# Optimization experiments

Measured on AMD Instinct MI355X. Metric: run time of the kernel, lower is better.

The kernel has to match this reference:

```python
import jax, jax.numpy as jnp
import numpy as np

N = 8192
E = 262144
H = 64


def setup_inputs() -> dict:
    key = jax.random.key(0)
    ks = jax.random.split(key, 9)
    edge_index = jax.random.randint(ks[0], (2, E), 0, N, dtype=jnp.int64)
    edge_attr = jax.random.uniform(ks[1], (E,), dtype=jnp.float32)
    node_features = jax.random.normal(ks[2], (N, N), dtype=jnp.float32)
    # GCNConv weights (glorot-ish scale) and biases
    W1 = jax.random.normal(ks[3], (N, H), dtype=jnp.float32) / np.sqrt(N)
    b1 = jnp.zeros((H,), dtype=jnp.float32)
    W2 = jax.random.normal(ks[4], (H, H), dtype=jnp.float32) / np.sqrt(H)
    b2 = jnp.zeros((H,), dtype=jnp.float32)
    fcW = jax.random.normal(ks[5], (H, N), dtype=jnp.float32) / np.sqrt(H)
    fcb = jnp.zeros((N,), dtype=jnp.float32)
    return {"edge_index": edge_index, "edge_attr": edge_attr,
            "node_features": node_features,
            "W1": W1, "b1": b1, "W2": W2, "b2": b2,
            "fcW": fcW, "fcb": fcb}


def _gcn_conv(x, W, b, src, dst, ew, n_nodes):
    # PyG GCNConv with edge weights: x' = D^{-1/2} (A + I) D^{-1/2} (x W) + b
    # src/dst/ew already include self-loops (weight 1.0).
    x = x @ W                                        # [N, out]
    deg = jax.ops.segment_sum(ew, dst, num_segments=n_nodes)  # in-degree w/ loops
    dinv = jax.lax.rsqrt(deg)                        # deg >= 1 due to self loops
    norm = dinv[src] * ew * dinv[dst]                # [E+N]
    out = jax.ops.segment_sum(x[src] * norm[:, None], dst, num_segments=n_nodes)
    return out + b


def reference(edge_index, edge_attr, node_features, W1, b1, W2, b2, fcW, fcb):
    n_nodes = node_features.shape[0]
    loops = jnp.arange(n_nodes, dtype=edge_index.dtype)
    src = jnp.concatenate([edge_index[0], loops])
    dst = jnp.concatenate([edge_index[1], loops])
    ew = jnp.concatenate([edge_attr, jnp.ones((n_nodes,), edge_attr.dtype)])
    x = jax.nn.relu(_gcn_conv(node_features, W1, b1, src, dst, ew, n_nodes))
    x = jax.nn.relu(_gcn_conv(x, W2, b2, src, dst, ew, n_nodes))
    x = x @ fcW + fcb
    return jax.nn.softmax(x, axis=-1)
```

## Files before the change

kernel.cpp:

```cpp
#include <hip/hip_runtime.h>


#define NN 8192
#define NE 262144
#define HD 64

typedef float f32x4 __attribute__((ext_vector_type(4)));
typedef short v8s   __attribute__((ext_vector_type(8)));
typedef unsigned short ushort_t;

__device__ __forceinline__ unsigned short bf16_rne(float f){
  union { float f; unsigned u; } v; v.f = f;
  unsigned r = v.u + 0x7fffu + ((v.u >> 16) & 1u);
  return (unsigned short)(r >> 16);
}
__device__ __forceinline__ float bf16_f32(unsigned short h){
  union { unsigned u; float f; } v; v.u = ((unsigned)h) << 16;
  return v.f;
}
__device__ __forceinline__ f32x4 mfma16(v8s a, v8s b, f32x4 c){
  return __builtin_amdgcn_mfma_f32_16x16x32_bf16(a, b, c, 0, 0, 0);
}

__global__ void k_init(float* deg, int* cnt, int* wcnt, float* S){
  int i = blockIdx.x*blockDim.x + threadIdx.x;
  if (i < NN){ deg[i]=1.0f; cnt[i]=0; wcnt[i]=0; S[i]=0.0f; }
}

__global__ void k_deg_cnt(const int* ei, const float* ew, float* deg, int* cnt){
  int e = blockIdx.x*blockDim.x + threadIdx.x;
  if (e < NE){
    int d = ei[NE + e];
    atomicAdd(&deg[d], ew[e]);
    atomicAdd(&cnt[d], 1);
  }
}

__global__ void k_dinv(const float* deg, float* dinv){
  int i = blockIdx.x*blockDim.x + threadIdx.x;
  if (i < NN) dinv[i] = 1.0f / sqrtf(deg[i]);
}

__global__ void k_scan(const int* cnt, int* rowptr){
  __shared__ int part[256];
  int t = threadIdx.x;
  int loc[32]; int s = 0;
  #pragma unroll
  for (int j=0;j<32;++j){ loc[j] = cnt[t*32+j]; s += loc[j]; }
  part[t] = s; __syncthreads();
  for (int off=1; off<256; off<<=1){
    int v = (t >= off) ? part[t-off] : 0;
    __syncthreads();
    part[t] += v;
    __syncthreads();
  }
  int run = part[t] - s;
  #pragma unroll
  for (int j=0;j<32;++j){ rowptr[t*32+j] = run; run += loc[j]; }
  if (t == 255) rowptr[NN] = run;
}

__global__ void k_fill(const int* ei, const float* ew, const float* dinv,
                       const int* rowptr, int* wcnt, int* csr_src, float* csr_nrm){
  int e = blockIdx.x*blockDim.x + threadIdx.x;
  if (e < NE){
    int s = ei[e], d = ei[NE+e];
    int slot = rowptr[d] + atomicAdd(&wcnt[d], 1);
    csr_src[slot] = s;
    csr_nrm[slot] = dinv[s] * ew[e] * dinv[d];
  }
}

__global__ void k_pack_w1(const float* W1, ushort_t* w1hi, ushort_t* w1lo){
  int idx = blockIdx.x*blockDim.x + threadIdx.x;
  if (idx < NN*HD){
    int kk = idx & 31, c = (idx>>5)&15, nt = (idx>>9)&3, kb = idx>>11;
    int k = kb*32 + kk, col = nt*16 + c;
    float w = W1[(size_t)k*HD + col];
    unsigned short hi = bf16_rne(w);
    w1hi[idx] = hi;
    w1lo[idx] = bf16_rne(w - bf16_f32(hi));
  }
}

__global__ void k_pack_fcw(const float* fcW, ushort_t* fcwp){
  int idx = blockIdx.x*blockDim.x + threadIdx.x;
  if (idx < HD*NN){
    int kk = idx & 31, c = (idx>>5)&15, cblk = (idx>>9)&511, kb = idx>>18;
    int k = kb*32 + kk, col = cblk*16 + c;
    fcwp[idx] = bf16_rne(fcW[(size_t)k*NN + col]);
  }
}

__global__ __launch_bounds__(512) void k_gemm1(const float* __restrict__ X,
                                               const ushort_t* __restrict__ w1hi,
                                               const ushort_t* __restrict__ w1lo,
                                               float* __restrict__ xw1){
  int tid = threadIdx.x, lane = tid & 63, w = tid >> 6;
  int r = lane & 15, seg = lane >> 4;
  int row0 = blockIdx.x * 32;
  const float* xr0 = X + (size_t)(row0 + r)     * NN + seg*8;
  const float* xr1 = X + (size_t)(row0 + 16 + r)* NN + seg*8;
  int kbase = w * 1024;

  f32x4 z = {0.f,0.f,0.f,0.f};
  f32x4 acc0[4] = {z,z,z,z};
  f32x4 acc1[4] = {z,z,z,z};

  f32x4 p00 = *(const f32x4*)(xr0 + kbase);
  f32x4 p01 = *(const f32x4*)(xr0 + kbase + 4);
  f32x4 p10 = *(const f32x4*)(xr1 + kbase);
  f32x4 p11 = *(const f32x4*)(xr1 + kbase + 4);

  for (int it = 0; it < 32; ++it){
    int k0 = kbase + it*32;
    int kb = k0 >> 5;
    f32x4 c00=p00, c01=p01, c10=p10, c11=p11;
    if (it < 31){
      int kn = k0 + 32;
      p00 = *(const f32x4*)(xr0 + kn);
      p01 = *(const f32x4*)(xr0 + kn + 4);
      p10 = *(const f32x4*)(xr1 + kn);
      p11 = *(const f32x4*)(xr1 + kn + 4);
    }
    v8s a0h, a0l, a1h, a1l;
    #pragma unroll
    for (int j=0;j<4;++j){
      float f = c00[j]; unsigned short h = bf16_rne(f);
      a0h[j] = (short)h; a0l[j] = (short)bf16_rne(f - bf16_f32(h));
      f = c01[j]; h = bf16_rne(f);
      a0h[4+j] = (short)h; a0l[4+j] = (short)bf16_rne(f - bf16_f32(h));
      f = c10[j]; h = bf16_rne(f);
      a1h[j] = (short)h; a1l[j] = (short)bf16_rne(f - bf16_f32(h));
      f = c11[j]; h = bf16_rne(f);
      a1h[4+j] = (short)h; a1l[4+j] = (short)bf16_rne(f - bf16_f32(h));
    }
    #pragma unroll
    for (int nt=0; nt<4; ++nt){
      size_t boff = ((size_t)(kb*4 + nt)*16 + r)*32 + seg*8;
      v8s bh = *(const v8s*)(w1hi + boff);
      v8s bl = *(const v8s*)(w1lo + boff);
      acc0[nt] = mfma16(a0h, bh, acc0[nt]);
      acc0[nt] = mfma16(a0h, bl, acc0[nt]);
      acc0[nt] = mfma16(a0l, bh, acc0[nt]);
      acc1[nt] = mfma16(a1h, bh, acc1[nt]);
      acc1[nt] = mfma16(a1h, bl, acc1[nt]);
      acc1[nt] = mfma16(a1l, bh, acc1[nt]);
    }
  }

  __shared__ float red[8][32][64];
  #pragma unroll
  for (int nt=0; nt<4; ++nt)
    #pragma unroll
    for (int j=0;j<4;++j){
      red[w][4*seg + j][nt*16 + r]      = acc0[nt][j];
      red[w][16 + 4*seg + j][nt*16 + r] = acc1[nt][j];
    }
  __syncthreads();
  for (int o = tid; o < 32*64; o += 512){
    int rr = o >> 6, cc = o & 63;
    float s = 0.f;
    #pragma unroll
    for (int ww=0; ww<8; ++ww) s += red[ww][rr][cc];
    xw1[(size_t)(row0 + rr)*HD + cc] = s;
  }
}

__global__ __launch_bounds__(256) void k_agg(const float* __restrict__ xin,
                                             const float* __restrict__ bias,
                                             const float* __restrict__ dinv,
                                             const int* __restrict__ rowptr,
                                             const int* __restrict__ csr_src,
                                             const float* __restrict__ csr_nrm,
                                             float* outf, ushort_t* outb, int mode){
  int lane = threadIdx.x & 63, w = threadIdx.x >> 6;
  int i = blockIdx.x*4 + w;
  float di = dinv[i];
  float acc = di*di * xin[(size_t)i*HD + lane];
  int e = rowptr[i], e1 = rowptr[i+1];
  for (; e + 1 < e1; e += 2){
    int s0 = csr_src[e], s1 = csr_src[e+1];
    float n0 = csr_nrm[e], n1 = csr_nrm[e+1];
    acc += n0 * xin[(size_t)s0*HD + lane];
    acc += n1 * xin[(size_t)s1*HD + lane];
  }
  if (e < e1) acc += csr_nrm[e] * xin[(size_t)csr_src[e]*HD + lane];
  float v = acc + bias[lane];
  v = v > 0.f ? v : 0.f;
  if (mode == 0) outf[(size_t)i*HD + lane] = v;
  else           outb[(size_t)i*HD + lane] = bf16_rne(v);
}

__global__ __launch_bounds__(64) void k_conv2(const float* __restrict__ x1a,
                                              const float* __restrict__ W2,
                                              float* __restrict__ x2w){
  int i = blockIdx.x, h = threadIdx.x;
  __shared__ float xs[64];
  xs[h] = x1a[(size_t)i*HD + h];
  __syncthreads();
  float acc = 0.f;
  #pragma unroll
  for (int k=0;k<64;++k) acc += xs[k] * W2[k*HD + h];
  x2w[(size_t)i*HD + h] = acc;
}

__global__ __launch_bounds__(256) void k_rowsum(const ushort_t* __restrict__ x2b,
                                                const ushort_t* __restrict__ fcwp,
                                                const float* __restrict__ fcb,
                                                float* __restrict__ S){
  int lane = threadIdx.x & 63, w = threadIdx.x >> 6;
  int r = lane & 15, seg = lane >> 4;
  int row0 = blockIdx.x*128 + w*32;
  const ushort_t* xb = x2b + (size_t)(row0 + r)*HD + seg*8;
  v8s a00 = *(const v8s*)(xb);
  v8s a01 = *(const v8s*)(xb + 32);
  v8s a10 = *(const v8s*)(xb + 16*HD);
  v8s a11 = *(const v8s*)(xb + 16*HD + 32);
  float rp0[4] = {0,0,0,0}, rp1[4] = {0,0,0,0};
  for (int cb=0; cb<4; ++cb){
    int colbase = blockIdx.y*256 + cb*64;
    f32x4 z = {0.f,0.f,0.f,0.f};
    f32x4 acc0[4] = {z,z,z,z}, acc1[4] = {z,z,z,z};
    #pragma unroll
    for (int nt=0; nt<4; ++nt){
      int cblk = (colbase >> 4) + nt;
      v8s bA = *(const v8s*)(fcwp + ((size_t)cblk*16 + r)*32 + seg*8);
      v8s bB = *(const v8s*)(fcwp + ((size_t)(512 + cblk)*16 + r)*32 + seg*8);
      acc0[nt] = mfma16(a00, bA, acc0[nt]);
      acc0[nt] = mfma16(a01, bB, acc0[nt]);
      acc1[nt] = mfma16(a10, bA, acc1[nt]);
      acc1[nt] = mfma16(a11, bB, acc1[nt]);
    }
    #pragma unroll
    for (int nt=0; nt<4; ++nt){
      int col = colbase + nt*16 + r;
      float fb = fcb[col];
      #pragma unroll
      for (int j=0;j<4;++j){
        rp0[j] += __expf(acc0[nt][j] + fb);
        rp1[j] += __expf(acc1[nt][j] + fb);
      }
    }
  }
  #pragma unroll
  for (int m=1; m<16; m<<=1)
    #pragma unroll
    for (int j=0;j<4;++j){
      rp0[j] += __shfl_xor(rp0[j], m);
      rp1[j] += __shfl_xor(rp1[j], m);
    }
  if (r == 0){
    #pragma unroll
    for (int j=0;j<4;++j){
      atomicAdd(&S[row0 + 4*seg + j],      rp0[j]);
      atomicAdd(&S[row0 + 16 + 4*seg + j], rp1[j]);
    }
  }
}

__global__ void k_sinv(const float* S, float* Sinv){
  int i = blockIdx.x*blockDim.x + threadIdx.x;
  if (i < NN) Sinv[i] = 1.0f / S[i];
}

__global__ __launch_bounds__(256) void k_passB(const ushort_t* __restrict__ x2b,
                                               const ushort_t* __restrict__ fcwp,
                                               const float* __restrict__ fcb,
                                               const float* __restrict__ Sinv,
                                               float* __restrict__ out){
  int lane = threadIdx.x & 63, w = threadIdx.x >> 6;
  int r = lane & 15, seg = lane >> 4;
  int row0 = blockIdx.x*128 + w*32;
  const ushort_t* xb = x2b + (size_t)(row0 + r)*HD + seg*8;
  v8s a00 = *(const v8s*)(xb);
  v8s a01 = *(const v8s*)(xb + 32);
  v8s a10 = *(const v8s*)(xb + 16*HD);
  v8s a11 = *(const v8s*)(xb + 16*HD + 32);
  float si0[4], si1[4];
  #pragma unroll
  for (int j=0;j<4;++j){
    si0[j] = Sinv[row0 + 4*seg + j];
    si1[j] = Sinv[row0 + 16 + 4*seg + j];
  }
  for (int cb=0; cb<4; ++cb){
    int colbase = blockIdx.y*256 + cb*64;
    f32x4 z = {0.f,0.f,0.f,0.f};
    f32x4 acc0[4] = {z,z,z,z}, acc1[4] = {z,z,z,z};
    #pragma unroll
    for (int nt=0; nt<4; ++nt){
      int cblk = (colbase >> 4) + nt;
      v8s bA = *(const v8s*)(fcwp + ((size_t)cblk*16 + r)*32 + seg*8);
      v8s bB = *(const v8s*)(fcwp + ((size_t)(512 + cblk)*16 + r)*32 + seg*8);
      acc0[nt] = mfma16(a00, bA, acc0[nt]);
      acc0[nt] = mfma16(a01, bB, acc0[nt]);
      acc1[nt] = mfma16(a10, bA, acc1[nt]);
      acc1[nt] = mfma16(a11, bB, acc1[nt]);
    }
    #pragma unroll
    for (int nt=0; nt<4; ++nt){
      int col = colbase + nt*16 + r;
      float fb = fcb[col];
      #pragma unroll
      for (int j=0;j<4;++j){
        out[(size_t)(row0 + 4*seg + j)*NN + col]      = __expf(acc0[nt][j] + fb) * si0[j];
        out[(size_t)(row0 + 16 + 4*seg + j)*NN + col] = __expf(acc1[nt][j] + fb) * si1[j];
      }
    }
  }
}

extern "C" void kernel_launch(void* const* d_in, const int* in_sizes, int n_in,
                              void* d_out, int out_size, void* d_ws, size_t ws_size,
                              hipStream_t stream){
  (void)in_sizes; (void)n_in; (void)out_size; (void)ws_size;
  const int*   ei  = (const int*)  d_in[0];
  const float* ew  = (const float*)d_in[1];
  const float* X   = (const float*)d_in[2];
  const float* W1  = (const float*)d_in[3];
  const float* b1  = (const float*)d_in[4];
  const float* W2  = (const float*)d_in[5];
  const float* b2  = (const float*)d_in[6];
  const float* fcW = (const float*)d_in[7];
  const float* fcb = (const float*)d_in[8];
  float* out = (float*)d_out;
  char*  ws  = (char*)d_ws;

  float*    deg     = (float*)   (ws + 0);
  float*    dinv    = (float*)   (ws + 32768);
  int*      cnt     = (int*)     (ws + 65536);
  int*      wcnt    = (int*)     (ws + 98304);
  int*      rowptr  = (int*)     (ws + 131072);
  int*      csr_src = (int*)     (ws + 167936);
  float*    csr_nrm = (float*)   (ws + 1216512);
  ushort_t* w1hi    = (ushort_t*)(ws + 2265088);
  ushort_t* w1lo    = (ushort_t*)(ws + 3313664);
  ushort_t* fcwp    = (ushort_t*)(ws + 4362240);
  float*    xw1     = (float*)   (ws + 5410816);
  float*    x1a     = (float*)   (ws + 7507968);
  float*    x2w     = (float*)   (ws + 9605120);
  ushort_t* x2b     = (ushort_t*)(ws + 11702272);
  float*    S       = (float*)   (ws + 12750848);
  float*    Sinv    = (float*)   (ws + 12783616);

  k_init    <<<32,   256, 0, stream>>>(deg, cnt, wcnt, S);
  k_deg_cnt <<<1024, 256, 0, stream>>>(ei, ew, deg, cnt);
  k_dinv    <<<32,   256, 0, stream>>>(deg, dinv);
  k_scan    <<<1,    256, 0, stream>>>(cnt, rowptr);
  k_fill    <<<1024, 256, 0, stream>>>(ei, ew, dinv, rowptr, wcnt, csr_src, csr_nrm);
  k_pack_w1 <<<2048, 256, 0, stream>>>(W1, w1hi, w1lo);
  k_pack_fcw<<<2048, 256, 0, stream>>>(fcW, fcwp);
  k_gemm1   <<<256,  512, 0, stream>>>(X, w1hi, w1lo, xw1);
  k_agg     <<<2048, 256, 0, stream>>>(xw1, b1, dinv, rowptr, csr_src, csr_nrm, x1a, (ushort_t*)0, 0);
  k_conv2   <<<8192,  64, 0, stream>>>(x1a, W2, x2w);
  k_agg     <<<2048, 256, 0, stream>>>(x2w, b2, dinv, rowptr, csr_src, csr_nrm, (float*)0, x2b, 1);
  k_rowsum  <<<dim3(64,32), 256, 0, stream>>>(x2b, fcwp, fcb, S);
  k_sinv    <<<32,   256, 0, stream>>>(S, Sinv);
  k_passB   <<<dim3(64,32), 256, 0, stream>>>(x2b, fcwp, fcb, Sinv, out);
}
```

Baseline: 301.4 us.

## Fuse small kernels, transpose MFMA operands for vectorized softmax stores

```diff
diff --git a/kernel.cpp b/kernel.cpp
--- a/kernel.cpp
+++ b/kernel.cpp
@@ -22,9 +22,24 @@
   return __builtin_amdgcn_mfma_f32_16x16x32_bf16(a, b, c, 0, 0, 0);
 }
 
-__global__ void k_init(float* deg, int* cnt, int* wcnt, float* S){
-  int i = blockIdx.x*blockDim.x + threadIdx.x;
-  if (i < NN){ deg[i]=1.0f; cnt[i]=0; wcnt[i]=0; S[i]=0.0f; }
+__global__ void k_prep0(const float* __restrict__ W1, const float* __restrict__ fcW,
+                        ushort_t* w1hi, ushort_t* w1lo, ushort_t* fcwp,
+                        float* deg, int* cnt, int* wcnt, float* S){
+  int idx = blockIdx.x*blockDim.x + threadIdx.x;
+  if (idx < NN){ deg[idx]=1.0f; cnt[idx]=0; wcnt[idx]=0; S[idx]=0.0f; }
+  {
+    int kk = idx & 31, c = (idx>>5)&15, nt = (idx>>9)&3, kb = idx>>11;
+    int k = kb*32 + kk, col = nt*16 + c;
+    float w = W1[(size_t)k*HD + col];
+    unsigned short hi = bf16_rne(w);
+    w1hi[idx] = hi;
+    w1lo[idx] = bf16_rne(w - bf16_f32(hi));
+  }
+  {
+    int kk = idx & 31, c = (idx>>5)&15, cblk = (idx>>9)&511, kb = idx>>18;
+    int k = kb*32 + kk, col = cblk*16 + c;
+    fcwp[idx] = bf16_rne(fcW[(size_t)k*NN + col]);
+  }
 }
 
 __global__ void k_deg_cnt(const int* ei, const float* ew, float* deg, int* cnt){
@@ -36,12 +51,7 @@
   }
 }
 
-__global__ void k_dinv(const float* deg, float* dinv){
-  int i = blockIdx.x*blockDim.x + threadIdx.x;
-  if (i < NN) dinv[i] = 1.0f / sqrtf(deg[i]);
-}
-
-__global__ void k_scan(const int* cnt, int* rowptr){
+__global__ void k_scan(const int* cnt, const float* deg, int* rowptr, float* dinv){
   __shared__ int part[256];
   int t = threadIdx.x;
   int loc[32]; int s = 0;
@@ -58,6 +68,8 @@
   #pragma unroll
   for (int j=0;j<32;++j){ rowptr[t*32+j] = run; run += loc[j]; }
   if (t == 255) rowptr[NN] = run;
+  #pragma unroll
+  for (int j=0;j<32;++j) dinv[t*32+j] = 1.0f / sqrtf(deg[t*32+j]);
 }
 
 __global__ void k_fill(const int* ei, const float* ew, const float* dinv,
@@ -68,27 +80,6 @@
     int slot = rowptr[d] + atomicAdd(&wcnt[d], 1);
     csr_src[slot] = s;
     csr_nrm[slot] = dinv[s] * ew[e] * dinv[d];
-  }
-}
-
-__global__ void k_pack_w1(const float* W1, ushort_t* w1hi, ushort_t* w1lo){
-  int idx = blockIdx.x*blockDim.x + threadIdx.x;
-  if (idx < NN*HD){
-    int kk = idx & 31, c = (idx>>5)&15, nt = (idx>>9)&3, kb = idx>>11;
-    int k = kb*32 + kk, col = nt*16 + c;
-    float w = W1[(size_t)k*HD + col];
-    unsigned short hi = bf16_rne(w);
-    w1hi[idx] = hi;
-    w1lo[idx] = bf16_rne(w - bf16_f32(hi));
-  }
-}
-
-__global__ void k_pack_fcw(const float* fcW, ushort_t* fcwp){
-  int idx = blockIdx.x*blockDim.x + threadIdx.x;
-  if (idx < HD*NN){
-    int kk = idx & 31, c = (idx>>5)&15, cblk = (idx>>9)&511, kb = idx>>18;
-    int k = kb*32 + kk, col = cblk*16 + c;
-    fcwp[idx] = bf16_rne(fcW[(size_t)k*NN + col]);
   }
 }
 
@@ -149,7 +140,7 @@
     }
   }
 
-  __shared__ float red[8][32][64];
+  __shared__ float red[8][32][65];
   #pragma unroll
   for (int nt=0; nt<4; ++nt)
     #pragma unroll
@@ -167,13 +158,48 @@
   }
 }
 
-__global__ __launch_bounds__(256) void k_agg(const float* __restrict__ xin,
-                                             const float* __restrict__ bias,
-                                             const float* __restrict__ dinv,
-                                             const int* __restrict__ rowptr,
-                                             const int* __restrict__ csr_src,
-                                             const float* __restrict__ csr_nrm,
-                                             float* outf, ushort_t* outb, int mode){
+__global__ __launch_bounds__(256) void k_agg1c(const float* __restrict__ xin,
+                                               const float* __restrict__ b1,
+                                               const float* __restrict__ W2,
+                                               const float* __restrict__ dinv,
+                                               const int* __restrict__ rowptr,
+                                               const int* __restrict__ csr_src,
+                                               const float* __restrict__ csr_nrm,
+                                               float* __restrict__ x2w){
+  __shared__ float W2s[64*64];
+  __shared__ float rows[4][64];
+  int lane = threadIdx.x & 63, w = threadIdx.x >> 6;
+  for (int o = threadIdx.x; o < 64*64; o += 256) W2s[o] = W2[o];
+  __syncthreads();
+
+  int i = blockIdx.x*4 + w;
+  float di = dinv[i];
+  float acc = di*di * xin[(size_t)i*HD + lane];
+  int e = rowptr[i], e1 = rowptr[i+1];
+  for (; e + 1 < e1; e += 2){
+    int s0 = csr_src[e], s1 = csr_src[e+1];
+    float n0 = csr_nrm[e], n1 = csr_nrm[e+1];
+    acc += n0 * xin[(size_t)s0*HD + lane];
+    acc += n1 * xin[(size_t)s1*HD + lane];
+  }
+  if (e < e1) acc += csr_nrm[e] * xin[(size_t)csr_src[e]*HD + lane];
+  float v = acc + b1[lane];
+  rows[w][lane] = v > 0.f ? v : 0.f;
+  __syncthreads();
+
+  float acc2 = 0.f;
+  #pragma unroll
+  for (int k=0;k<64;++k) acc2 += rows[w][k] * W2s[k*64 + lane];
+  x2w[(size_t)i*HD + lane] = acc2;
+}
+
+__global__ __launch_bounds__(256) void k_agg2(const float* __restrict__ xin,
+                                              const float* __restrict__ b2,
+                                              const float* __restrict__ dinv,
+                                              const int* __restrict__ rowptr,
+                                              const int* __restrict__ csr_src,
+                                              const float* __restrict__ csr_nrm,
+                                              ushort_t* __restrict__ x2b){
   int lane = threadIdx.x & 63, w = threadIdx.x >> 6;
   int i = blockIdx.x*4 + w;
   float di = dinv[i];
@@ -186,23 +212,9 @@
     acc += n1 * xin[(size_t)s1*HD + lane];
   }
   if (e < e1) acc += csr_nrm[e] * xin[(size_t)csr_src[e]*HD + lane];
-  float v = acc + bias[lane];
+  float v = acc + b2[lane];
   v = v > 0.f ? v : 0.f;
-  if (mode == 0) outf[(size_t)i*HD + lane] = v;
-  else           outb[(size_t)i*HD + lane] = bf16_rne(v);
-}
-
-__global__ __launch_bounds__(64) void k_conv2(const float* __restrict__ x1a,
-                                              const float* __restrict__ W2,
-                                              float* __restrict__ x2w){
-  int i = blockIdx.x, h = threadIdx.x;
-  __shared__ float xs[64];
-  xs[h] = x1a[(size_t)i*HD + h];
-  __syncthreads();
-  float acc = 0.f;
-  #pragma unroll
-  for (int k=0;k<64;++k) acc += xs[k] * W2[k*HD + h];
-  x2w[(size_t)i*HD + h] = acc;
+  x2b[(size_t)i*HD + lane] = bf16_rne(v);
 }
 
 __global__ __launch_bounds__(256) void k_rowsum(const ushort_t* __restrict__ x2b,
@@ -213,11 +225,11 @@
   int r = lane & 15, seg = lane >> 4;
   int row0 = blockIdx.x*128 + w*32;
   const ushort_t* xb = x2b + (size_t)(row0 + r)*HD + seg*8;
-  v8s a00 = *(const v8s*)(xb);
-  v8s a01 = *(const v8s*)(xb + 32);
-  v8s a10 = *(const v8s*)(xb + 16*HD);
-  v8s a11 = *(const v8s*)(xb + 16*HD + 32);
-  float rp0[4] = {0,0,0,0}, rp1[4] = {0,0,0,0};
+  v8s x00 = *(const v8s*)(xb);
+  v8s x01 = *(const v8s*)(xb + 32);
+  v8s x10 = *(const v8s*)(xb + 16*HD);
+  v8s x11 = *(const v8s*)(xb + 16*HD + 32);
+  float rp0 = 0.f, rp1 = 0.f;
   for (int cb=0; cb<4; ++cb){
     int colbase = blockIdx.y*256 + cb*64;
     f32x4 z = {0.f,0.f,0.f,0.f};
@@ -227,62 +239,47 @@
       int cblk = (colbase >> 4) + nt;
       v8s bA = *(const v8s*)(fcwp + ((size_t)cblk*16 + r)*32 + seg*8);
       v8s bB = *(const v8s*)(fcwp + ((size_t)(512 + cblk)*16 + r)*32 + seg*8);
-      acc0[nt] = mfma16(a00, bA, acc0[nt]);
-      acc0[nt] = mfma16(a01, bB, acc0[nt]);
-      acc1[nt] = mfma16(a10, bA, acc1[nt]);
-      acc1[nt] = mfma16(a11, bB, acc1[nt]);
-    }
-    #pragma unroll
-    for (int nt=0; nt<4; ++nt){
-      int col = colbase + nt*16 + r;
-      float fb = fcb[col];
+      acc0[nt] = mfma16(bA, x00, acc0[nt]);
+      acc0[nt] = mfma16(bB, x01, acc0[nt]);
+      acc1[nt] = mfma16(bA, x10, acc1[nt]);
+      acc1[nt] = mfma16(bB, x11, acc1[nt]);
+    }
+    #pragma unroll
+    for (int nt=0; nt<4; ++nt){
+      int col = colbase + nt*16 + seg*4;
+      f32x4 fb = *(const f32x4*)(fcb + col);
       #pragma unroll
       for (int j=0;j<4;++j){
-        rp0[j] += __expf(acc0[nt][j] + fb);
-        rp1[j] += __expf(acc1[nt][j] + fb);
+        rp0 += __expf(acc0[nt][j] + fb[j]);
+        rp1 += __expf(acc1[nt][j] + fb[j]);
       }
     }
   }
-  #pragma unroll
-  for (int m=1; m<16; m<<=1)
-    #pragma unroll
-    for (int j=0;j<4;++j){
-      rp0[j] += __shfl_xor(rp0[j], m);
-      rp1[j] += __shfl_xor(rp1[j], m);
-    }
-  if (r == 0){
-    #pragma unroll
-    for (int j=0;j<4;++j){
-      atomicAdd(&S[row0 + 4*seg + j],      rp0[j]);
-      atomicAdd(&S[row0 + 16 + 4*seg + j], rp1[j]);
-    }
-  }
-}
-
-__global__ void k_sinv(const float* S, float* Sinv){
-  int i = blockIdx.x*blockDim.x + threadIdx.x;
-  if (i < NN) Sinv[i] = 1.0f / S[i];
+  rp0 += __shfl_xor(rp0, 16); rp0 += __shfl_xor(rp0, 32);
+  rp1 += __shfl_xor(rp1, 16); rp1 += __shfl_xor(rp1, 32);
+  if (lane < 16){
+    atomicAdd(&S[row0 + lane],      rp0);
+    atomicAdd(&S[row0 + 16 + lane], rp1);
+  }
 }
 
 __global__ __launch_bounds__(256) void k_passB(const ushort_t* __restrict__ x2b,
                                                const ushort_t* __restrict__ fcwp,
                                                const float* __restrict__ fcb,
-                                               const float* __restrict__ Sinv,
+                                               const float* __restrict__ S,
                                                float* __restrict__ out){
   int lane = threadIdx.x & 63, w = threadIdx.x >> 6;
   int r = lane & 15, seg = lane >> 4;
   int row0 = blockIdx.x*128 + w*32;
   const ushort_t* xb = x2b + (size_t)(row0 + r)*HD + seg*8;
-  v8s a00 = *(const v8s*)(xb);
-  v8s a01 = *(const v8s*)(xb + 32);
-  v8s a10 = *(const v8s*)(xb + 16*HD);
-  v8s a11 = *(const v8s*)(xb + 16*HD + 32);
-  float si0[4], si1[4];
-  #pragma unroll
-  for (int j=0;j<4;++j){
-    si0[j] = Sinv[row0 + 4*seg + j];
-    si1[j] = Sinv[row0 + 16 + 4*seg + j];
-  }
+  v8s x00 = *(const v8s*)(xb);
+  v8s x01 = *(const v8s*)(xb + 32);
+  v8s x10 = *(const v8s*)(xb + 16*HD);
+  v8s x11 = *(const v8s*)(xb + 16*HD + 32);
+  float si0 = 1.0f / S[row0 + r];
+  float si1 = 1.0f / S[row0 + 16 + r];
+  float* o0 = out + (size_t)(row0 + r)*NN;
+  float* o1 = out + (size_t)(row0 + 16 + r)*NN;
   for (int cb=0; cb<4; ++cb){
     int colbase = blockIdx.y*256 + cb*64;
     f32x4 z = {0.f,0.f,0.f,0.f};
@@ -292,20 +289,23 @@
       int cblk = (colbase >> 4) + nt;
       v8s bA = *(const v8s*)(fcwp + ((size_t)cblk*16 + r)*32 + seg*8);
       v8s bB = *(const v8s*)(fcwp + ((size_t)(512 + cblk)*16 + r)*32 + seg*8);
-      acc0[nt] = mfma16(a00, bA, acc0[nt]);
-      acc0[nt] = mfma16(a01, bB, acc0[nt]);
-      acc1[nt] = mfma16(a10, bA, acc1[nt]);
-      acc1[nt] = mfma16(a11, bB, acc1[nt]);
-    }
-    #pragma unroll
-    for (int nt=0; nt<4; ++nt){
-      int col = colbase + nt*16 + r;
-      float fb = fcb[col];
+      acc0[nt] = mfma16(bA, x00, acc0[nt]);
+      acc0[nt] = mfma16(bB, x01, acc0[nt]);
+      acc1[nt] = mfma16(bA, x10, acc1[nt]);
+      acc1[nt] = mfma16(bB, x11, acc1[nt]);
+    }
+    #pragma unroll
+    for (int nt=0; nt<4; ++nt){
+      int col = colbase + nt*16 + seg*4;
+      f32x4 fb = *(const f32x4*)(fcb + col);
+      f32x4 v0, v1;
       #pragma unroll
       for (int j=0;j<4;++j){
-        out[(size_t)(row0 + 4*seg + j)*NN + col]      = __expf(acc0[nt][j] + fb) * si0[j];
-        out[(size_t)(row0 + 16 + 4*seg + j)*NN + col] = __expf(acc1[nt][j] + fb) * si1[j];
+        v0[j] = __expf(acc0[nt][j] + fb[j]) * si0;
+        v1[j] = __expf(acc1[nt][j] + fb[j]) * si1;
       }
+      *(f32x4*)(o0 + col) = v0;
+      *(f32x4*)(o1 + col) = v1;
     }
   }
 }
@@ -337,24 +337,17 @@
   ushort_t* w1lo    = (ushort_t*)(ws + 3313664);
   ushort_t* fcwp    = (ushort_t*)(ws + 4362240);
   float*    xw1     = (float*)   (ws + 5410816);
-  float*    x1a     = (float*)   (ws + 7507968);
-  float*    x2w     = (float*)   (ws + 9605120);
-  ushort_t* x2b     = (ushort_t*)(ws + 11702272);
-  float*    S       = (float*)   (ws + 12750848);
-  float*    Sinv    = (float*)   (ws + 12783616);
-
-  k_init    <<<32,   256, 0, stream>>>(deg, cnt, wcnt, S);
+  float*    x2w     = (float*)   (ws + 7507968);
+  ushort_t* x2b     = (ushort_t*)(ws + 9605120);
+  float*    S       = (float*)   (ws + 10653696);
+
+  k_prep0   <<<2048, 256, 0, stream>>>(W1, fcW, w1hi, w1lo, fcwp, deg, cnt, wcnt, S);
   k_deg_cnt <<<1024, 256, 0, stream>>>(ei, ew, deg, cnt);
-  k_dinv    <<<32,   256, 0, stream>>>(deg, dinv);
-  k_scan    <<<1,    256, 0, stream>>>(cnt, rowptr);
+  k_scan    <<<1,    256, 0, stream>>>(cnt, deg, rowptr, dinv);
   k_fill    <<<1024, 256, 0, stream>>>(ei, ew, dinv, rowptr, wcnt, csr_src, csr_nrm);
-  k_pack_w1 <<<2048, 256, 0, stream>>>(W1, w1hi, w1lo);
-  k_pack_fcw<<<2048, 256, 0, stream>>>(fcW, fcwp);
   k_gemm1   <<<256,  512, 0, stream>>>(X, w1hi, w1lo, xw1);
-  k_agg     <<<2048, 256, 0, stream>>>(xw1, b1, dinv, rowptr, csr_src, csr_nrm, x1a, (ushort_t*)0, 0);
-  k_conv2   <<<8192,  64, 0, stream>>>(x1a, W2, x2w);
-  k_agg     <<<2048, 256, 0, stream>>>(x2w, b2, dinv, rowptr, csr_src, csr_nrm, (float*)0, x2b, 1);
+  k_agg1c   <<<2048, 256, 0, stream>>>(xw1, b1, W2, dinv, rowptr, csr_src, csr_nrm, x2w);
+  k_agg2    <<<2048, 256, 0, stream>>>(x2w, b2, dinv, rowptr, csr_src, csr_nrm, x2b);
   k_rowsum  <<<dim3(64,32), 256, 0, stream>>>(x2b, fcwp, fcb, S);
-  k_sinv    <<<32,   256, 0, stream>>>(S, Sinv);
-  k_passB   <<<dim3(64,32), 256, 0, stream>>>(x2b, fcwp, fcb, Sinv, out);
-}
+  k_passB   <<<dim3(64,32), 256, 0, stream>>>(x2b, fcwp, fcb, S, out);
+}
```

Measured after the change: 300.3 us. About the same (-0.4%).
